# Optimization experiments

Hardware: AMD Instinct MI355X
Metric: run time of the kernel (lower is better)

## Reference

```python
import jax, jax.numpy as jnp
import numpy as np

NUM_CLASSES = 10
TAU = 3.3333333


def thermometer_encode(x, thresholds):
    # x: [B, F], thresholds: [F, T] -> binary bits [B, F*T]
    bits = (x[:, :, None] > thresholds[None, :, :]).astype(x.dtype)
    B = x.shape[0]
    return bits.reshape(B, -1)


def lut_layer(h, idx, luts):
    # h: [B, I] activations in [0,1]; idx: [O, n] input mapping; luts: [O, 2^n]
    # Multilinear interpolation over the 2^n LUT corners (gather + fold).
    xs = h[:, idx]                       # [B, O, n] gathered inputs
    B, O, n = xs.shape
    acc = jnp.broadcast_to(luts[None, :, :], (B, O, luts.shape[1]))  # [B, O, 2^n]
    for k in range(n):                   # fold one input bit per step (MSB first)
        half = acc.shape[-1] // 2
        xk = xs[:, :, k:k + 1]           # [B, O, 1]
        acc = acc[..., :half] * (1.0 - xk) + acc[..., half:] * xk
    return acc[..., 0]                   # [B, O]


def group_sum(h, k, tau):
    # h: [B, W] -> [B, k] popcount-style grouped sum scaled by 1/tau
    B, W = h.shape
    return h.reshape(B, k, W // k).sum(axis=-1) / tau


def setup_inputs() -> dict:
    key = jax.random.key(0)
    ks = jax.random.split(key, 6)
    B, F, T = 512, 1024, 3
    I = F * T                            # 3072 thermometer bits
    O1, O2, n = 2000, 1000, 6
    x = jax.random.normal(ks[0], (B, F), dtype=jnp.float32)
    thresholds = jax.random.normal(ks[1], (F, T), dtype=jnp.float32)
    luts1 = jax.random.uniform(ks[2], (O1, 2 ** n), dtype=jnp.float32)
    idx1 = jax.random.randint(ks[3], (O1, n), 0, I, dtype=jnp.int32)
    luts2 = jax.random.uniform(ks[4], (O2, 2 ** n), dtype=jnp.float32)
    idx2 = jax.random.randint(ks[5], (O2, n), 0, O1, dtype=jnp.int32)
    return {"x": x, "thresholds": thresholds, "luts1": luts1, "idx1": idx1,
            "luts2": luts2, "idx2": idx2}


def reference(x, thresholds, luts1, idx1, luts2, idx2):
    h = thermometer_encode(x, thresholds)     # [B, 3072] binary
    h = lut_layer(h, idx1, luts1)             # [B, 2000]
    h = lut_layer(h, idx2, luts2)             # [B, 1000]
    return group_sum(h, NUM_CLASSES, TAU)     # [B, 10]
```

## Files before the change

### kernel.cpp

```cpp
#include <hip/hip_runtime.h>


#define BATCH 512
#define FEAT  1024
#define NTHR  3
#define NBITS (FEAT * NTHR)
#define O1    2000
#define O2    1000
#define NCLS  10

__global__ __launch_bounds__(256) void dwn_fused(
    const float* __restrict__ x,
    const float* __restrict__ thr,
    const float* __restrict__ luts1,
    const int*   __restrict__ idx1,
    const float* __restrict__ luts2,
    const int*   __restrict__ idx2,
    float* __restrict__ out)
{
    __shared__ unsigned char s_bits[NBITS];
    __shared__ float s_h1[O1];
    __shared__ float s_h2[O2];

    const int b = blockIdx.x;
    const int t = threadIdx.x;

    for (int f = t; f < FEAT; f += 256) {
        float xv = x[b * FEAT + f];
        s_bits[f * 3 + 0] = (unsigned char)(xv > thr[f * 3 + 0]);
        s_bits[f * 3 + 1] = (unsigned char)(xv > thr[f * 3 + 1]);
        s_bits[f * 3 + 2] = (unsigned char)(xv > thr[f * 3 + 2]);
    }
    __syncthreads();

    for (int o = t; o < O1; o += 256) {
        const int* ip = idx1 + o * 6;
        int code = 0;
#pragma unroll
        for (int k = 0; k < 6; ++k)
            code |= ((int)s_bits[ip[k]]) << (5 - k);
        s_h1[o] = luts1[o * 64 + code];
    }
    __syncthreads();

    for (int o = t; o < O2; o += 256) {
        const int* ip = idx2 + o * 6;
        float xv0 = s_h1[ip[0]];
        float xv1 = s_h1[ip[1]];
        float xv2 = s_h1[ip[2]];
        float xv3 = s_h1[ip[3]];
        float xv4 = s_h1[ip[4]];
        float xv5 = s_h1[ip[5]];

        const float4* lp = (const float4*)(luts2 + (size_t)o * 64);
        float v[16];
#pragma unroll
        for (int q = 0; q < 16; ++q) {
            float4 e = lp[q];
            float u0 = e.x + xv5 * (e.y - e.x);
            float u1 = e.z + xv5 * (e.w - e.z);
            v[q] = u0 + xv4 * (u1 - u0);
        }
#pragma unroll
        for (int q = 0; q < 8; ++q) v[q] = v[2*q] + xv3 * (v[2*q+1] - v[2*q]);
#pragma unroll
        for (int q = 0; q < 4; ++q) v[q] = v[2*q] + xv2 * (v[2*q+1] - v[2*q]);
#pragma unroll
        for (int q = 0; q < 2; ++q) v[q] = v[2*q] + xv1 * (v[2*q+1] - v[2*q]);
        s_h2[o] = v[0] + xv0 * (v[1] - v[0]);
    }
    __syncthreads();

    if (t < NCLS) {
        float s = 0.0f;
#pragma unroll 4
        for (int j = 0; j < 100; ++j) s += s_h2[t * 100 + j];
        out[b * NCLS + t] = s / 3.3333333f;
    }
}

extern "C" void kernel_launch(void* const* d_in, const int* in_sizes, int n_in,
                              void* d_out, int out_size, void* d_ws, size_t ws_size,
                              hipStream_t stream) {
    const float* x      = (const float*)d_in[0];
    const float* thr    = (const float*)d_in[1];
    const float* luts1  = (const float*)d_in[2];
    const int*   idx1   = (const int*)  d_in[3];
    const float* luts2  = (const float*)d_in[4];
    const int*   idx2   = (const int*)  d_in[5];
    float* out = (float*)d_out;

    dwn_fused<<<BATCH, 256, 0, stream>>>(x, thr, luts1, idx1, luts2, idx2, out);
}
```

Baseline: 87.05 us.

## Process two batch rows per block to share index and LUT loads

Each block now handles two batch rows with 512 threads. Adjacent threads share the same output neuron, so the idx and LUT global loads are reused across rows, and index reads are vectorized as int2. The final group sum becomes a two-level parallel reduction instead of 10 serial threads. The costs are a doubled shared-memory footprint, fewer blocks (256), and possibly lower occupancy.

```diff
diff --git a/kernel.cpp b/kernel.cpp
--- a/kernel.cpp
+++ b/kernel.cpp
@@ -3,13 +3,14 @@
 
 #define BATCH 512
 #define FEAT  1024
-#define NTHR  3
-#define NBITS (FEAT * NTHR)
+#define NBITS (FEAT * 3)
 #define O1    2000
 #define O2    1000
 #define NCLS  10
+#define G     2
+#define NT    512
 
-__global__ __launch_bounds__(256) void dwn_fused(
+__global__ __launch_bounds__(NT) void dwn_fused2(
     const float* __restrict__ x,
     const float* __restrict__ thr,
     const float* __restrict__ luts1,
@@ -18,39 +19,48 @@
     const int*   __restrict__ idx2,
     float* __restrict__ out)
 {
-    __shared__ unsigned char s_bits[NBITS];
-    __shared__ float s_h1[O1];
-    __shared__ float s_h2[O2];
+    __shared__ unsigned char s_bits[G][NBITS];
+    __shared__ float s_h1[G][O1];
+    __shared__ float s_h2[G][O2];
+    __shared__ float s_part[G * NCLS * 10];
 
-    const int b = blockIdx.x;
-    const int t = threadIdx.x;
+    const int b0 = blockIdx.x * G;
+    const int t  = threadIdx.x;
 
-    for (int f = t; f < FEAT; f += 256) {
-        float xv = x[b * FEAT + f];
-        s_bits[f * 3 + 0] = (unsigned char)(xv > thr[f * 3 + 0]);
-        s_bits[f * 3 + 1] = (unsigned char)(xv > thr[f * 3 + 1]);
-        s_bits[f * 3 + 2] = (unsigned char)(xv > thr[f * 3 + 2]);
+    for (int i = t; i < G * FEAT; i += NT) {
+        int r = i >> 10;
+        int f = i & (FEAT - 1);
+        float xv = x[(b0 + r) * FEAT + f];
+        const float* tp = thr + f * 3;
+        s_bits[r][f * 3 + 0] = (unsigned char)(xv > tp[0]);
+        s_bits[r][f * 3 + 1] = (unsigned char)(xv > tp[1]);
+        s_bits[r][f * 3 + 2] = (unsigned char)(xv > tp[2]);
     }
     __syncthreads();
 
-    for (int o = t; o < O1; o += 256) {
-        const int* ip = idx1 + o * 6;
-        int code = 0;
-#pragma unroll
-        for (int k = 0; k < 6; ++k)
-            code |= ((int)s_bits[ip[k]]) << (5 - k);
-        s_h1[o] = luts1[o * 64 + code];
+    for (int i = t; i < G * O1; i += NT) {
+        int o = i >> 1;
+        int r = i & 1;
+        const int2* ip = (const int2*)(idx1 + o * 6);
+        int2 p0 = ip[0], p1 = ip[1], p2 = ip[2];
+        int code = ((int)s_bits[r][p0.x] << 5) | ((int)s_bits[r][p0.y] << 4)
+                 | ((int)s_bits[r][p1.x] << 3) | ((int)s_bits[r][p1.y] << 2)
+                 | ((int)s_bits[r][p2.x] << 1) |  (int)s_bits[r][p2.y];
+        s_h1[r][o] = luts1[o * 64 + code];
     }
     __syncthreads();
 
-    for (int o = t; o < O2; o += 256) {
-        const int* ip = idx2 + o * 6;
-        float xv0 = s_h1[ip[0]];
-        float xv1 = s_h1[ip[1]];
-        float xv2 = s_h1[ip[2]];
-        float xv3 = s_h1[ip[3]];
-        float xv4 = s_h1[ip[4]];
-        float xv5 = s_h1[ip[5]];
+    for (int i = t; i < G * O2; i += NT) {
+        int o = i >> 1;
+        int r = i & 1;
+        const int2* ip = (const int2*)(idx2 + o * 6);
+        int2 p0 = ip[0], p1 = ip[1], p2 = ip[2];
+        float xv0 = s_h1[r][p0.x];
+        float xv1 = s_h1[r][p0.y];
+        float xv2 = s_h1[r][p1.x];
+        float xv3 = s_h1[r][p1.y];
+        float xv4 = s_h1[r][p2.x];
+        float xv5 = s_h1[r][p2.y];
 
         const float4* lp = (const float4*)(luts2 + (size_t)o * 64);
         float v[16];
@@ -67,15 +77,29 @@
         for (int q = 0; q < 4; ++q) v[q] = v[2*q] + xv2 * (v[2*q+1] - v[2*q]);
 #pragma unroll
         for (int q = 0; q < 2; ++q) v[q] = v[2*q] + xv1 * (v[2*q+1] - v[2*q]);
-        s_h2[o] = v[0] + xv0 * (v[1] - v[0]);
+        s_h2[r][o] = v[0] + xv0 * (v[1] - v[0]);
     }
     __syncthreads();
 
-    if (t < NCLS) {
+    if (t < G * NCLS * 10) {
+        int g = t / 10;
+        int p = t % 10;
+        int r   = g / NCLS;
+        int cls = g % NCLS;
+        const float* hp = &s_h2[r][cls * 100 + p * 10];
         float s = 0.0f;
-#pragma unroll 4
-        for (int j = 0; j < 100; ++j) s += s_h2[t * 100 + j];
-        out[b * NCLS + t] = s / 3.3333333f;
+#pragma unroll
+        for (int j = 0; j < 10; ++j) s += hp[j];
+        s_part[t] = s;
+    }
+    __syncthreads();
+    if (t < G * NCLS) {
+        float s = 0.0f;
+#pragma unroll
+        for (int j = 0; j < 10; ++j) s += s_part[t * 10 + j];
+        int r   = t / NCLS;
+        int cls = t % NCLS;
+        out[(b0 + r) * NCLS + cls] = s / 3.3333333f;
     }
 }
 
@@ -90,5 +114,5 @@
     const int*   idx2   = (const int*)  d_in[5];
     float* out = (float*)d_out;
 
-    dwn_fused<<<BATCH, 256, 0, stream>>>(x, thr, luts1, idx1, luts2, idx2, out);
+    dwn_fused2<<<BATCH / G, NT, 0, stream>>>(x, thr, luts1, idx1, luts2, idx2, out);
 }
```

New measurement: 79.61 us. 8.5% less time.
